# Optimization experiments

Measured on AMD Instinct MI355X. Metric: run time of the kernel, lower is better.

Reference implementation:

```python
import jax, jax.numpy as jnp
import numpy as np

B, T, DP, DQ, DO = 128, 2048, 256, 256, 256


def setup_inputs() -> dict:
    key = jax.random.key(0)
    ks = jax.random.split(key, 10)
    return {
        "input_p": jax.random.normal(ks[0], (B, DP), dtype=jnp.float32),
        "mask_p": jnp.ones((B,), dtype=jnp.float32),
        "input_q": jax.random.normal(ks[1], (B, T, DQ), dtype=jnp.float32),
        "mask_q": jax.random.randint(ks[2], (B, T), 0, 2, dtype=jnp.int32),
        "h_tm1": jax.random.normal(ks[3], (B, DO), dtype=jnp.float32),
        # layer-0 parameters (depth == 0)
        "W_p_r": jax.random.normal(ks[4], (DO, DP + DO), dtype=jnp.float32) * 0.04,
        "b_p_r": jnp.zeros((DO,), dtype=jnp.float32),
        "W_q": jax.random.normal(ks[5], (DO, DQ), dtype=jnp.float32) * 0.05,
        "b_q": jnp.zeros((DO,), dtype=jnp.float32),
        "w": jax.random.normal(ks[6], (DO,), dtype=jnp.float32) * 0.05,
        "match_b": jnp.ones((1,), dtype=jnp.float32),
        "depth": 0,
    }


def masked_softmax(x, m, axis=-1):
    x = jnp.clip(x, -15.0, 15.0)
    x = x * m
    e_x = jnp.exp(x - jnp.max(x, axis=axis, keepdims=True))
    e_x = e_x * m
    return e_x / (jnp.sum(e_x, axis=axis, keepdims=True) + 1e-6)


def reference(input_p, mask_p, input_q, mask_q, h_tm1, W_p_r, b_p_r, W_q, b_q, w, match_b, depth):
    mq = mask_q.astype(jnp.float32)
    # G_p_r: [B, 1, DO]
    G_p_r = (jnp.concatenate([input_p, h_tm1], axis=-1) @ W_p_r.T + b_p_r)[:, None, :]
    # G_q: [B, T, DO]
    G_q = input_q @ W_q.T + b_q
    G = jnp.tanh(G_p_r + G_q)
    alpha = jnp.einsum("btd,d->bt", G, w) + match_b  # [B, T]
    alpha = masked_softmax(alpha, mq, axis=-1)
    z = jnp.einsum("bt,btd->bd", alpha, input_q)  # bmm context
    return jnp.concatenate([input_p, z], axis=1)  # [B, DP+DQ]
```

## Files before the change

kernel.cpp:

```cpp
#include <hip/hip_runtime.h>
#include <hip/hip_bf16.h>

typedef short short8 __attribute__((ext_vector_type(8)));
typedef float floatx4 __attribute__((ext_vector_type(4)));

constexpr int Bn = 128, Tn = 2048, DPn = 256, DQn = 256, DOn = 256;
constexpr int NCH = Tn / 64;

__device__ inline unsigned pk2(float x, float y) {
    __hip_bfloat162 h = __float22bfloat162_rn(make_float2(x, y));
    return *(unsigned*)&h;
}
__device__ inline float fast_tanh(float x) {
    float e = __expf(2.0f * x);
    return 1.0f - 2.0f / (e + 1.0f);
}

__global__ __launch_bounds__(256) void cvt_wq_kernel(const float* __restrict__ wq,
                                                     unsigned short* __restrict__ wqbf) {
    int idx = blockIdx.x * 256 + threadIdx.x;
    float4 v = ((const float4*)wq)[idx];
    ((uint2*)wqbf)[idx] = make_uint2(pk2(v.x, v.y), pk2(v.z, v.w));
}

__global__ __launch_bounds__(256) void base_kernel(const float* __restrict__ input_p,
                                                   const float* __restrict__ h_tm1,
                                                   const float* __restrict__ Wpr,
                                                   const float* __restrict__ bpr,
                                                   const float* __restrict__ bq,
                                                   float* __restrict__ base) {
    __shared__ float v[512];
    int b = blockIdx.x, tid = threadIdx.x;
    v[tid]       = input_p[b * DPn + tid];
    v[256 + tid] = h_tm1[b * DOn + tid];
    __syncthreads();
    const float4* row = (const float4*)(Wpr + (size_t)tid * 512);
    const float4* vv  = (const float4*)v;
    float acc = 0.f;
#pragma unroll 8
    for (int i = 0; i < 128; i++) {
        float4 r = row[i], x = vv[i];
        acc = fmaf(r.x, x.x, acc);
        acc = fmaf(r.y, x.y, acc);
        acc = fmaf(r.z, x.z, acc);
        acc = fmaf(r.w, x.w, acc);
    }
    base[b * DOn + tid] = acc + bpr[tid] + bq[tid];
}

__global__ __launch_bounds__(256, 2) void fused_kernel(const float* __restrict__ q,
                                                       const unsigned short* __restrict__ wqbf,
                                                       const float* __restrict__ base,
                                                       const float* __restrict__ wvec,
                                                       const float* __restrict__ matchb,
                                                       const int* __restrict__ maskq,
                                                       float* __restrict__ zpart,
                                                       float* __restrict__ spart,
                                                       float* __restrict__ mpart) {
    __shared__ __align__(16) char shraw[32 * 64 * 16];
    unsigned short* qtile = (unsigned short*)shraw;
    __shared__ float partl[4][64];
    __shared__ float earr[64];

    int b = blockIdx.y, c = blockIdx.x;
    int t0 = c * 64;
    int tid = threadIdx.x;
    int w = tid >> 6, lane = tid & 63, l15 = lane & 15, quad = lane >> 4;

    short8 bfr[4][8];
    const unsigned short* bbase = wqbf + (size_t)(w * 64 + l15) * 256 + quad * 8;
#pragma unroll
    for (int nt = 0; nt < 4; nt++)
#pragma unroll
        for (int ks = 0; ks < 8; ks++)
            bfr[nt][ks] = *(const short8*)(bbase + nt * 16 * 256 + ks * 32);
    float bn[4], wn[4];
#pragma unroll
    for (int nt = 0; nt < 4; nt++) {
        int n = w * 64 + nt * 16 + l15;
        bn[nt] = base[b * DOn + n];
        wn[nt] = wvec[n];
    }

    {
        const float* src = q + ((size_t)b * Tn + t0 + w * 16 + l15) * DQn + quad * 8;
        unsigned short* dst = qtile + ((size_t)(w * 8) * 64 + lane) * 8;
#pragma unroll
        for (int ks = 0; ks < 8; ks++) {
            float4 v0 = *(const float4*)(src + ks * 32);
            float4 v1 = *(const float4*)(src + ks * 32 + 4);
            uint4 u;
            u.x = pk2(v0.x, v0.y);
            u.y = pk2(v0.z, v0.w);
            u.z = pk2(v1.x, v1.y);
            u.w = pk2(v1.z, v1.w);
            *(uint4*)(dst + ks * 512) = u;
        }
    }
    __syncthreads();

#pragma unroll
    for (int mt = 0; mt < 4; mt++) {
        short8 af[8];
        const unsigned short* ab = qtile + ((size_t)(mt * 8) * 64 + lane) * 8;
#pragma unroll
        for (int ks = 0; ks < 8; ks++) af[ks] = *(const short8*)(ab + ks * 512);
        float prow[4] = {0.f, 0.f, 0.f, 0.f};
#pragma unroll
        for (int nt = 0; nt < 4; nt++) {
            floatx4 acc = {0.f, 0.f, 0.f, 0.f};
#pragma unroll
            for (int ks = 0; ks < 8; ks++)
                acc = __builtin_amdgcn_mfma_f32_16x16x32_bf16(af[ks], bfr[nt][ks], acc, 0, 0, 0);
#pragma unroll
            for (int r = 0; r < 4; r++) {
                float g = fast_tanh(acc[r] + bn[nt]);
                prow[r] = fmaf(g, wn[nt], prow[r]);
            }
        }
#pragma unroll
        for (int off = 1; off < 16; off <<= 1)
#pragma unroll
            for (int r = 0; r < 4; r++) prow[r] += __shfl_xor(prow[r], off);
        if (l15 == 0) {
#pragma unroll
            for (int r = 0; r < 4; r++) partl[w][mt * 16 + quad * 4 + r] = prow[r];
        }
    }
    __syncthreads();

    if (tid < 64) {
        int t = tid;
        float lg = partl[0][t] + partl[1][t] + partl[2][t] + partl[3][t] + matchb[0];
        float m = (float)maskq[(size_t)b * Tn + t0 + t];
        float x = fminf(fmaxf(lg, -15.f), 15.f) * m;
        float e = __expf(x - 15.f) * m;
        earr[t] = e;
        float xm = x, es = e;
#pragma unroll
        for (int off = 1; off < 64; off <<= 1) {
            xm = fmaxf(xm, __shfl_xor(xm, off));
            es += __shfl_xor(es, off);
        }
        if (t == 0) {
            mpart[b * NCH + c] = xm;
            spart[b * NCH + c] = es;
        }
    }
    __syncthreads();

    {
        int o = lane & 31, h = lane >> 5, g = w * 2 + h;
        const float* qz = q + ((size_t)b * Tn + t0 + g * 8) * DQn + o * 8;
        float acc[8] = {0.f, 0.f, 0.f, 0.f, 0.f, 0.f, 0.f, 0.f};
#pragma unroll
        for (int s = 0; s < 8; s++) {
            float e = earr[g * 8 + s];
            float4 a0 = *(const float4*)(qz + (size_t)s * DQn);
            float4 a1 = *(const float4*)(qz + (size_t)s * DQn + 4);
            acc[0] = fmaf(e, a0.x, acc[0]);
            acc[1] = fmaf(e, a0.y, acc[1]);
            acc[2] = fmaf(e, a0.z, acc[2]);
            acc[3] = fmaf(e, a0.w, acc[3]);
            acc[4] = fmaf(e, a1.x, acc[4]);
            acc[5] = fmaf(e, a1.y, acc[5]);
            acc[6] = fmaf(e, a1.z, acc[6]);
            acc[7] = fmaf(e, a1.w, acc[7]);
        }
        float* zp = (float*)shraw;
        float* zrow = zp + g * 256 + o * 8;
        *(float4*)(zrow)     = make_float4(acc[0], acc[1], acc[2], acc[3]);
        *(float4*)(zrow + 4) = make_float4(acc[4], acc[5], acc[6], acc[7]);
    }
    __syncthreads();
    {
        const float* zp = (const float*)shraw;
        float zs = 0.f;
#pragma unroll
        for (int r = 0; r < 8; r++) zs += zp[r * 256 + tid];
        zpart[((size_t)b * NCH + c) * DQn + tid] = zs;
    }
}

__global__ __launch_bounds__(256) void final_kernel(const float* __restrict__ input_p,
                                                    const float* __restrict__ zpart,
                                                    const float* __restrict__ spart,
                                                    const float* __restrict__ mpart,
                                                    float* __restrict__ out) {
    int b = blockIdx.x, tid = threadIdx.x;
    float S = 0.f, mx = -1e30f;
#pragma unroll 8
    for (int c = 0; c < NCH; c++) {
        S += spart[b * NCH + c];
        mx = fmaxf(mx, mpart[b * NCH + c]);
    }
    float denom = S + 1e-6f * __expf(mx - 15.f);
    float inv = 1.0f / denom;
    float zs = 0.f;
#pragma unroll 8
    for (int c = 0; c < NCH; c++) zs += zpart[((size_t)b * NCH + c) * DQn + tid];
    out[(size_t)b * 512 + tid] = input_p[(size_t)b * DPn + tid];
    out[(size_t)b * 512 + 256 + tid] = zs * inv;
}

extern "C" void kernel_launch(void* const* d_in, const int* in_sizes, int n_in,
                              void* d_out, int out_size, void* d_ws, size_t ws_size,
                              hipStream_t stream) {
    const float* input_p = (const float*)d_in[0];
    const float* input_q = (const float*)d_in[2];
    const int*   mask_q  = (const int*)d_in[3];
    const float* h_tm1   = (const float*)d_in[4];
    const float* W_p_r   = (const float*)d_in[5];
    const float* b_p_r   = (const float*)d_in[6];
    const float* W_q     = (const float*)d_in[7];
    const float* b_q     = (const float*)d_in[8];
    const float* w       = (const float*)d_in[9];
    const float* match_b = (const float*)d_in[10];
    float* out = (float*)d_out;

    char* ws = (char*)d_ws;
    unsigned short* wqbf = (unsigned short*)ws;
    float* base  = (float*)(ws + 131072);
    float* zpart = (float*)(ws + 262144);
    float* spart = (float*)(ws + 262144 + 4194304);
    float* mpart = (float*)(ws + 262144 + 4194304 + 16384);

    cvt_wq_kernel<<<64, 256, 0, stream>>>(W_q, wqbf);
    base_kernel<<<Bn, 256, 0, stream>>>(input_p, h_tm1, W_p_r, b_p_r, b_q, base);
    fused_kernel<<<dim3(NCH, Bn), 256, 0, stream>>>(input_q, wqbf, base, w, match_b,
                                                    mask_q, zpart, spart, mpart);
    final_kernel<<<Bn, 256, 0, stream>>>(input_p, zpart, spart, mpart, out);
}
```

Baseline: 440.5 us.

## Stage fp32 q tile in swizzled LDS and reuse for MFMA and context sum

Loads each 64-row fp32 q tile into shared memory once with a coalesced, XOR-swizzled layout, converting to bf16 on the fly for the MFMA operands and reusing the same tile for the weighted context reduction instead of rereading q from global memory. Also merges the W_q conversion and base projection kernels into one launch. The tile raises shared memory per block to about 70KB, which may lower occupancy.

```diff
diff --git a/kernel.cpp b/kernel.cpp
--- a/kernel.cpp
+++ b/kernel.cpp
@@ -16,21 +16,23 @@
     return 1.0f - 2.0f / (e + 1.0f);
 }
 
-__global__ __launch_bounds__(256) void cvt_wq_kernel(const float* __restrict__ wq,
-                                                     unsigned short* __restrict__ wqbf) {
-    int idx = blockIdx.x * 256 + threadIdx.x;
-    float4 v = ((const float4*)wq)[idx];
-    ((uint2*)wqbf)[idx] = make_uint2(pk2(v.x, v.y), pk2(v.z, v.w));
-}
-
-__global__ __launch_bounds__(256) void base_kernel(const float* __restrict__ input_p,
+__global__ __launch_bounds__(256) void prep_kernel(const float* __restrict__ wq,
+                                                   unsigned short* __restrict__ wqbf,
+                                                   const float* __restrict__ input_p,
                                                    const float* __restrict__ h_tm1,
                                                    const float* __restrict__ Wpr,
                                                    const float* __restrict__ bpr,
                                                    const float* __restrict__ bq,
                                                    float* __restrict__ base) {
     __shared__ float v[512];
-    int b = blockIdx.x, tid = threadIdx.x;
+    int tid = threadIdx.x;
+    if (blockIdx.x < 64) {
+        int idx = blockIdx.x * 256 + tid;
+        float4 x = ((const float4*)wq)[idx];
+        ((uint2*)wqbf)[idx] = make_uint2(pk2(x.x, x.y), pk2(x.z, x.w));
+        return;
+    }
+    int b = blockIdx.x - 64;
     v[tid]       = input_p[b * DPn + tid];
     v[256 + tid] = h_tm1[b * DOn + tid];
     __syncthreads();
@@ -57,8 +59,8 @@
                                                        float* __restrict__ zpart,
                                                        float* __restrict__ spart,
                                                        float* __restrict__ mpart) {
-    __shared__ __align__(16) char shraw[32 * 64 * 16];
-    unsigned short* qtile = (unsigned short*)shraw;
+    __shared__ __align__(16) float tile[64 * 256];
+    __shared__ __align__(16) float zp[4][256];
     __shared__ float partl[4][64];
     __shared__ float earr[64];
 
@@ -66,6 +68,17 @@
     int t0 = c * 64;
     int tid = threadIdx.x;
     int w = tid >> 6, lane = tid & 63, l15 = lane & 15, quad = lane >> 4;
+    char* tb = (char*)tile;
+
+    {
+        const float* qsrc = q + ((size_t)b * Tn + t0) * DQn;
+#pragma unroll
+        for (int i = 0; i < 16; i++) {
+            int r = w * 16 + i;
+            float4 x = *(const float4*)(qsrc + (size_t)r * DQn + lane * 4);
+            *(float4*)(tb + r * 1024 + ((lane * 16) ^ ((r & 7) << 4))) = x;
+        }
+    }
 
     short8 bfr[4][8];
     const unsigned short* bbase = wqbf + (size_t)(w * 64 + l15) * 256 + quad * 8;
@@ -81,30 +94,26 @@
         bn[nt] = base[b * DOn + n];
         wn[nt] = wvec[n];
     }
-
-    {
-        const float* src = q + ((size_t)b * Tn + t0 + w * 16 + l15) * DQn + quad * 8;
-        unsigned short* dst = qtile + ((size_t)(w * 8) * 64 + lane) * 8;
+    __syncthreads();
+
+#pragma unroll
+    for (int mt = 0; mt < 4; mt++) {
+        int r = mt * 16 + l15;
+        const char* ab = tb + r * 1024;
+        int swz = (r & 7) << 4;
+        short8 af[8];
 #pragma unroll
         for (int ks = 0; ks < 8; ks++) {
-            float4 v0 = *(const float4*)(src + ks * 32);
-            float4 v1 = *(const float4*)(src + ks * 32 + 4);
-            uint4 u;
-            u.x = pk2(v0.x, v0.y);
-            u.y = pk2(v0.z, v0.w);
-            u.z = pk2(v1.x, v1.y);
-            u.w = pk2(v1.z, v1.w);
-            *(uint4*)(dst + ks * 512) = u;
-        }
-    }
-    __syncthreads();
-
-#pragma unroll
-    for (int mt = 0; mt < 4; mt++) {
-        short8 af[8];
-        const unsigned short* ab = qtile + ((size_t)(mt * 8) * 64 + lane) * 8;
-#pragma unroll
-        for (int ks = 0; ks < 8; ks++) af[ks] = *(const short8*)(ab + ks * 512);
+            int cb = quad * 32 + ks * 128;
+            float4 f0 = *(const float4*)(ab + (cb ^ swz));
+            float4 f1 = *(const float4*)(ab + ((cb + 16) ^ swz));
+            union { unsigned u[4]; short8 s; } cv;
+            cv.u[0] = pk2(f0.x, f0.y);
+            cv.u[1] = pk2(f0.z, f0.w);
+            cv.u[2] = pk2(f1.x, f1.y);
+            cv.u[3] = pk2(f1.z, f1.w);
+            af[ks] = cv.s;
+        }
         float prow[4] = {0.f, 0.f, 0.f, 0.f};
 #pragma unroll
         for (int nt = 0; nt < 4; nt++) {
@@ -113,18 +122,18 @@
             for (int ks = 0; ks < 8; ks++)
                 acc = __builtin_amdgcn_mfma_f32_16x16x32_bf16(af[ks], bfr[nt][ks], acc, 0, 0, 0);
 #pragma unroll
-            for (int r = 0; r < 4; r++) {
-                float g = fast_tanh(acc[r] + bn[nt]);
-                prow[r] = fmaf(g, wn[nt], prow[r]);
+            for (int rr = 0; rr < 4; rr++) {
+                float g = fast_tanh(acc[rr] + bn[nt]);
+                prow[rr] = fmaf(g, wn[nt], prow[rr]);
             }
         }
 #pragma unroll
         for (int off = 1; off < 16; off <<= 1)
 #pragma unroll
-            for (int r = 0; r < 4; r++) prow[r] += __shfl_xor(prow[r], off);
+            for (int rr = 0; rr < 4; rr++) prow[rr] += __shfl_xor(prow[rr], off);
         if (l15 == 0) {
 #pragma unroll
-            for (int r = 0; r < 4; r++) partl[w][mt * 16 + quad * 4 + r] = prow[r];
+            for (int rr = 0; rr < 4; rr++) partl[w][mt * 16 + quad * 4 + rr] = prow[rr];
         }
     }
     __syncthreads();
@@ -150,34 +159,22 @@
     __syncthreads();
 
     {
-        int o = lane & 31, h = lane >> 5, g = w * 2 + h;
-        const float* qz = q + ((size_t)b * Tn + t0 + g * 8) * DQn + o * 8;
-        float acc[8] = {0.f, 0.f, 0.f, 0.f, 0.f, 0.f, 0.f, 0.f};
-#pragma unroll
-        for (int s = 0; s < 8; s++) {
-            float e = earr[g * 8 + s];
-            float4 a0 = *(const float4*)(qz + (size_t)s * DQn);
-            float4 a1 = *(const float4*)(qz + (size_t)s * DQn + 4);
-            acc[0] = fmaf(e, a0.x, acc[0]);
-            acc[1] = fmaf(e, a0.y, acc[1]);
-            acc[2] = fmaf(e, a0.z, acc[2]);
-            acc[3] = fmaf(e, a0.w, acc[3]);
-            acc[4] = fmaf(e, a1.x, acc[4]);
-            acc[5] = fmaf(e, a1.y, acc[5]);
-            acc[6] = fmaf(e, a1.z, acc[6]);
-            acc[7] = fmaf(e, a1.w, acc[7]);
-        }
-        float* zp = (float*)shraw;
-        float* zrow = zp + g * 256 + o * 8;
-        *(float4*)(zrow)     = make_float4(acc[0], acc[1], acc[2], acc[3]);
-        *(float4*)(zrow + 4) = make_float4(acc[4], acc[5], acc[6], acc[7]);
+        float a0 = 0.f, a1 = 0.f, a2 = 0.f, a3 = 0.f;
+#pragma unroll
+        for (int i = 0; i < 16; i++) {
+            int r = w * 16 + i;
+            float e = earr[r];
+            float4 x = *(const float4*)(tb + r * 1024 + ((lane * 16) ^ ((r & 7) << 4)));
+            a0 = fmaf(e, x.x, a0);
+            a1 = fmaf(e, x.y, a1);
+            a2 = fmaf(e, x.z, a2);
+            a3 = fmaf(e, x.w, a3);
+        }
+        *(float4*)&zp[w][lane * 4] = make_float4(a0, a1, a2, a3);
     }
     __syncthreads();
     {
-        const float* zp = (const float*)shraw;
-        float zs = 0.f;
-#pragma unroll
-        for (int r = 0; r < 8; r++) zs += zp[r * 256 + tid];
+        float zs = zp[0][tid] + zp[1][tid] + zp[2][tid] + zp[3][tid];
         zpart[((size_t)b * NCH + c) * DQn + tid] = zs;
     }
 }
@@ -225,8 +222,7 @@
     float* spart = (float*)(ws + 262144 + 4194304);
     float* mpart = (float*)(ws + 262144 + 4194304 + 16384);
 
-    cvt_wq_kernel<<<64, 256, 0, stream>>>(W_q, wqbf);
-    base_kernel<<<Bn, 256, 0, stream>>>(input_p, h_tm1, W_p_r, b_p_r, b_q, base);
+    prep_kernel<<<192, 256, 0, stream>>>(W_q, wqbf, input_p, h_tm1, W_p_r, b_p_r, b_q, base);
     fused_kernel<<<dim3(NCH, Bn), 256, 0, stream>>>(input_q, wqbf, base, w, match_b,
                                                     mask_q, zpart, spart, mpart);
     final_kernel<<<Bn, 256, 0, stream>>>(input_p, zpart, spart, mpart, out);
```

After: 427.9 us. -2.9%, faster.
